# Performance work log

Measured on AMD Instinct MI355X. Metric: run time of the kernel, lower is better.

## Reference

```python
import jax, jax.numpy as jnp
import numpy as np

B, C, D, H, W = 8, 256, 128, 64, 64


def setup_inputs() -> dict:
    key = jax.random.key(0)
    ks = jax.random.split(key, 7)
    s = 1.0 / np.sqrt(C)
    return {
        "q": jax.random.normal(ks[0], (B, C, H, W), dtype=jnp.float32),
        "k": jax.random.normal(ks[1], (B, C, H, W), dtype=jnp.float32),
        "v": jax.random.normal(ks[2], (B, C, H, W), dtype=jnp.float32),
        "W_theta": jax.random.normal(ks[3], (D, C), dtype=jnp.float32) * s,
        "W_phi": jax.random.normal(ks[4], (D, C), dtype=jnp.float32) * s,
        "W_g": jax.random.normal(ks[5], (D, C), dtype=jnp.float32) * s,
        "W_out": jax.random.normal(ks[6], (C, D), dtype=jnp.float32) * (1.0 / np.sqrt(D)),
    }


def reference(q, k, v, W_theta, W_phi, W_g, W_out):
    # 1x1 conv projections (no bias) == channel matmuls
    b, c, h, w = q.shape
    d = W_theta.shape[0]
    n = h * w
    qp = jnp.einsum('bchw,dc->bhwd', q, W_theta).reshape(b, n, d)   # [B,N,d]
    kp = jnp.einsum('bchw,dc->bhwd', k, W_phi).reshape(b, n, d)     # [B,N,d]
    vp = jnp.einsum('bchw,dc->bhwd', v, W_g).reshape(b, n, d)       # [B,N,d]
    # embedded_gaussian: scores / sqrt(d), softmax over dim=1 (query axis!)
    scores = jnp.einsum('bnd,bmd->bnm', qp, kp) / jnp.sqrt(jnp.asarray(d, qp.dtype))
    attn = jax.nn.softmax(scores, axis=1)                           # NOTE: axis=1, matches torch dim=1
    out = jnp.einsum('bnm,bmd->bnd', attn, vp).reshape(b, h, w, d)  # [B,H,W,d]
    out = jnp.einsum('bhwd,cd->bchw', out, W_out)                   # conv_out 1x1
    return v + out
```

## Files before the change

kernel.cpp:

```cpp
#include <hip/hip_runtime.h>
#include <stdint.h>

#define B_ 8
#define C_ 256
#define D_ 128
#define N_ 4096

typedef __bf16 bf16x8 __attribute__((ext_vector_type(8)));
typedef uint16_t u16x8 __attribute__((ext_vector_type(8)));
typedef uint16_t u16x4 __attribute__((ext_vector_type(4)));
typedef float f32x4 __attribute__((ext_vector_type(4)));
typedef uint32_t u32x2 __attribute__((ext_vector_type(2)));

__device__ inline uint16_t f2bf(float x) {
    union { float f; uint32_t u; } v; v.f = x;
    uint32_t u = v.u;
    return (uint16_t)((u + 0x7FFFu + ((u >> 16) & 1u)) >> 16);
}

__device__ inline float bf2f(uint16_t v) {
    union { uint32_t u; float f; } x; x.u = (uint32_t)v << 16; return x.f;
}

__device__ inline uint32_t pkbf(float lo, float hi) {
    __bf16 l = (__bf16)lo, h = (__bf16)hi;
    uint16_t lu = __builtin_bit_cast(uint16_t, l);
    uint16_t hu = __builtin_bit_cast(uint16_t, h);
    return ((uint32_t)hu << 16) | (uint32_t)lu;
}

__device__ inline float dexp2(float x) { return __builtin_amdgcn_exp2f(x); }

__global__ __launch_bounds__(256) void prep_weights(
    const float* __restrict__ wt, const float* __restrict__ wp,
    const float* __restrict__ wg, const float* __restrict__ wo,
    uint16_t* __restrict__ bwt, uint16_t* __restrict__ bwp,
    uint16_t* __restrict__ bwg, uint16_t* __restrict__ bwo)
{
    int i = blockIdx.x * 256 + threadIdx.x;
    const float scale = 0.127517431f;
    bwt[i] = f2bf(wt[i] * scale);
    bwp[i] = f2bf(wp[i]);
    bwg[i] = f2bf(wg[i]);
    bwo[i] = f2bf(wo[i]);
}

__global__ __launch_bounds__(256) void proj_kernel(
    const float* __restrict__ q, const float* __restrict__ k, const float* __restrict__ v,
    const uint16_t* __restrict__ bwt, const uint16_t* __restrict__ bwp, const uint16_t* __restrict__ bwg,
    uint16_t* __restrict__ qp, uint16_t* __restrict__ kp, uint16_t* __restrict__ vpT)
{
    const int which = blockIdx.z;
    const float* src = (which == 0) ? q : ((which == 1) ? k : v);
    const uint16_t* w = (which == 0) ? bwt : ((which == 1) ? bwp : bwg);
    const int b   = blockIdx.y;
    const int n0  = blockIdx.x * 64;
    const int wav = threadIdx.x >> 6;
    const int lane = threadIdx.x & 63;
    const int col = lane & 15;
    const int quad = lane >> 4;
    const int n = n0 + wav * 16 + col;

    const float* srcb = src + (size_t)b * C_ * N_;

    f32x4 acc[8];
#pragma unroll
    for (int mf = 0; mf < 8; ++mf) acc[mf] = (f32x4){0.f, 0.f, 0.f, 0.f};

    for (int kc = 0; kc < 8; ++kc) {
        const int cbase = kc * 32 + quad * 8;
        u16x8 bb;
#pragma unroll
        for (int j = 0; j < 8; ++j)
            bb[j] = f2bf(srcb[(size_t)(cbase + j) * N_ + n]);
        bf16x8 bfrag = __builtin_bit_cast(bf16x8, bb);
#pragma unroll
        for (int mf = 0; mf < 8; ++mf) {
            bf16x8 afrag = *(const bf16x8*)(w + (size_t)(mf * 16 + col) * C_ + cbase);
            acc[mf] = __builtin_amdgcn_mfma_f32_16x16x32_bf16(afrag, bfrag, acc[mf], 0, 0, 0);
        }
    }

    if (which < 2) {
        uint16_t* dst = (which == 0) ? qp : kp;
        uint16_t* base = dst + ((size_t)b * N_ + n) * D_;
#pragma unroll
        for (int mf = 0; mf < 8; ++mf) {
            u16x4 pk;
#pragma unroll
            for (int r = 0; r < 4; ++r) pk[r] = f2bf(acc[mf][r]);
            *(u16x4*)(base + mf * 16 + quad * 4) = pk;
        }
    } else {
        uint16_t* base = vpT + (size_t)b * D_ * N_;
#pragma unroll
        for (int mf = 0; mf < 8; ++mf)
#pragma unroll
            for (int r = 0; r < 4; ++r) {
                int d = mf * 16 + quad * 4 + r;
                base[(size_t)d * N_ + n] = f2bf(acc[mf][r]);
            }
    }
}

__global__ __launch_bounds__(256) void pass1_denom(
    const uint16_t* __restrict__ qp, const uint16_t* __restrict__ kp,
    float* __restrict__ part)
{
    const int b  = blockIdx.x & 7;
    const int mt = (blockIdx.x >> 3) & 31;
    const int ns = blockIdx.x >> 8;
    const int m0 = mt * 128;
    const int wav = threadIdx.x >> 6;
    const int lane = threadIdx.x & 63;
    const int c = lane & 15;
    const int q = lane >> 4;

    const uint16_t* qpb = qp + (size_t)b * N_ * D_;
    const uint16_t* kpb = kp + (size_t)b * N_ * D_;

    bf16x8 bfr[8][4];
#pragma unroll
    for (int mf = 0; mf < 8; ++mf)
#pragma unroll
        for (int kc = 0; kc < 4; ++kc)
            bfr[mf][kc] = *(const bf16x8*)(kpb + (size_t)(m0 + mf * 16 + c) * D_ + kc * 32 + q * 8);

    float colsum[8];
#pragma unroll
    for (int mf = 0; mf < 8; ++mf) colsum[mf] = 0.f;

    for (int it = 0; it < 32; ++it) {
        const int nbase = ns * 2048 + it * 64 + wav * 16;
        bf16x8 afr[4];
#pragma unroll
        for (int kc = 0; kc < 4; ++kc)
            afr[kc] = *(const bf16x8*)(qpb + (size_t)(nbase + c) * D_ + kc * 32 + q * 8);
#pragma unroll
        for (int mf = 0; mf < 8; ++mf) {
            f32x4 acc = (f32x4){0.f, 0.f, 0.f, 0.f};
#pragma unroll
            for (int kc = 0; kc < 4; ++kc)
                acc = __builtin_amdgcn_mfma_f32_16x16x32_bf16(afr[kc], bfr[mf][kc], acc, 0, 0, 0);
#pragma unroll
            for (int r = 0; r < 4; ++r)
                colsum[mf] += dexp2(acc[r]);
        }
    }

    __shared__ float cs[4][128];
#pragma unroll
    for (int mf = 0; mf < 8; ++mf) {
        float s = colsum[mf];
        s += __shfl_down(s, 16, 64);
        s += __shfl_down(s, 32, 64);
        if (q == 0) cs[wav][mf * 16 + c] = s;
    }
    __syncthreads();
    if (threadIdx.x < 128) {
        float s = cs[0][threadIdx.x] + cs[1][threadIdx.x] + cs[2][threadIdx.x] + cs[3][threadIdx.x];
        part[((size_t)ns * 8 + b) * N_ + m0 + threadIdx.x] = s;
    }
}

__global__ __launch_bounds__(256) void scale_vpt(
    const float* __restrict__ part, uint16_t* __restrict__ vpT)
{
    const size_t base = ((size_t)blockIdx.x * 256 + threadIdx.x) * 8;
    const int b = (int)(base >> 19);
    const int m = (int)(base & (N_ - 1));
    const float* p0 = part + (size_t)b * N_ + m;
    const float* p1 = part + (size_t)(8 + b) * N_ + m;
    u16x8 v = *(const u16x8*)(vpT + base);
    u16x8 r;
#pragma unroll
    for (int j = 0; j < 8; ++j) {
        float inv = __builtin_amdgcn_rcpf(p0[j] + p1[j]);
        r[j] = f2bf(bf2f(v[j]) * inv);
    }
    *(u16x8*)(vpT + base) = r;
}

__global__ __launch_bounds__(256, 2) void pass2_attn(
    const uint16_t* __restrict__ qp, const uint16_t* __restrict__ kp,
    const uint16_t* __restrict__ vpT,
    uint16_t* __restrict__ ob0, uint16_t* __restrict__ ob1,
    uint16_t* __restrict__ ob2, uint16_t* __restrict__ ob3)
{
    const int b   = blockIdx.x & 7;
    const int qtr = (blockIdx.x >> 3) & 3;
    const int nsb = blockIdx.x >> 5;
    const int wav = threadIdx.x >> 6;
    const int lane = threadIdx.x & 63;
    const int c = lane & 15;
    const int q = lane >> 4;
    const int ntile = nsb * 256 + wav * 64;

    const uint16_t* qpb = qp + (size_t)b * N_ * D_;
    const uint16_t* kpb = kp + (size_t)b * N_ * D_;
    const uint16_t* vtb = vpT + (size_t)b * D_ * N_;

    __shared__ __align__(16) uint16_t stage[2][8192];
    __shared__ __align__(16) uint16_t plds[4][4][16][72];

#define STAGE(bufidx, m0_)                                                          \
    {                                                                               \
        uint16_t* lb = &stage[bufidx][0];                                           \
        _Pragma("unroll")                                                           \
        for (int j = 0; j < 4; ++j) {                                               \
            const int fid = wav * 4 + j;                                            \
            const uint16_t* g;                                                      \
            uint16_t* ld;                                                           \
            if (fid < 8) {                                                          \
                const int P = fid * 64 + lane;                                      \
                const int mm = P >> 4, js = P & 15;                                 \
                const int jj = js ^ (mm & 7);                                       \
                g = kpb + (size_t)((m0_) + mm) * D_ + jj * 8;                       \
                ld = lb + fid * 512;                                                \
            } else {                                                                \
                const int P = (fid - 8) * 64 + lane;                                \
                const int dd = P >> 2, js = P & 3;                                  \
                const int jj = js ^ ((dd >> 1) & 3);                                \
                g = vtb + (size_t)dd * N_ + (m0_) + jj * 8;                         \
                ld = lb + 4096 + (fid - 8) * 512;                                   \
            }                                                                       \
            __builtin_amdgcn_global_load_lds(                                       \
                (const __attribute__((address_space(1))) unsigned int*)g,           \
                (__attribute__((address_space(3))) unsigned int*)ld,                \
                16, 0, 0);                                                          \
        }                                                                           \
    }

    bf16x8 qfr[4][4];
#pragma unroll
    for (int nf = 0; nf < 4; ++nf)
#pragma unroll
        for (int kc = 0; kc < 4; ++kc)
            qfr[nf][kc] = *(const bf16x8*)(qpb + (size_t)(ntile + nf * 16 + c) * D_ + kc * 32 + q * 8);

    f32x4 oacc[4][8];
#pragma unroll
    for (int nf = 0; nf < 4; ++nf)
#pragma unroll
        for (int df = 0; df < 8; ++df) oacc[nf][df] = (f32x4){0.f, 0.f, 0.f, 0.f};

    const int mstart = qtr * (N_ / 4);
    STAGE(0, mstart);
    __syncthreads();

    for (int ch = 0; ch < 32; ++ch) {
        const int m0 = mstart + ch * 32;
        const int cur = ch & 1;
        STAGE(cur ^ 1, mstart + ((ch + 1) & 31) * 32);

        const uint16_t* sb = &stage[cur][0];

        bf16x8 kf[2][4];
#pragma unroll
        for (int mf = 0; mf < 2; ++mf)
#pragma unroll
            for (int kc = 0; kc < 4; ++kc) {
                const int js = (kc * 4 + q) ^ (c & 7);
                kf[mf][kc] = *(const bf16x8*)(sb + (mf * 16 + c) * 128 + js * 8);
            }

        __builtin_amdgcn_s_setprio(1);
#pragma unroll
        for (int nf = 0; nf < 4; ++nf) {
            f32x4 s0 = (f32x4){0.f, 0.f, 0.f, 0.f};
            f32x4 s1 = (f32x4){0.f, 0.f, 0.f, 0.f};
#pragma unroll
            for (int kc = 0; kc < 4; ++kc)
                s0 = __builtin_amdgcn_mfma_f32_16x16x32_bf16(kf[0][kc], qfr[nf][kc], s0, 0, 0, 0);
#pragma unroll
            for (int kc = 0; kc < 4; ++kc)
                s1 = __builtin_amdgcn_mfma_f32_16x16x32_bf16(kf[1][kc], qfr[nf][kc], s1, 0, 0, 0);
            uint32_t p00 = pkbf(dexp2(s0[0]), dexp2(s0[1]));
            uint32_t p01 = pkbf(dexp2(s0[2]), dexp2(s0[3]));
            uint32_t p10 = pkbf(dexp2(s1[0]), dexp2(s1[1]));
            uint32_t p11 = pkbf(dexp2(s1[2]), dexp2(s1[3]));
            uint16_t* row = &plds[wav][nf][c][0];
            *(u32x2*)(row + 4 * q)      = (u32x2){p00, p01};
            *(u32x2*)(row + 16 + 4 * q) = (u32x2){p10, p11};
        }
        __builtin_amdgcn_s_setprio(0);

        const int vjs = q ^ ((c >> 1) & 3);
        bf16x8 vf[8];
#pragma unroll
        for (int df = 0; df < 8; ++df)
            vf[df] = *(const bf16x8*)(sb + 4096 + (df * 16 + c) * 32 + vjs * 8);

        bf16x8 pf[4];
#pragma unroll
        for (int nf = 0; nf < 4; ++nf)
            pf[nf] = *(const bf16x8*)(&plds[wav][nf][c][8 * q]);

        __builtin_amdgcn_s_setprio(1);
#pragma unroll
        for (int nf = 0; nf < 4; ++nf)
#pragma unroll
            for (int df = 0; df < 8; ++df)
                oacc[nf][df] = __builtin_amdgcn_mfma_f32_16x16x32_bf16(pf[nf], vf[df], oacc[nf][df], 0, 0, 0);
        __builtin_amdgcn_s_setprio(0);

        __syncthreads();
    }
#undef STAGE

    uint16_t* obq = (qtr == 0) ? ob0 : (qtr == 1) ? ob1 : (qtr == 2) ? ob2 : ob3;
#pragma unroll
    for (int nf = 0; nf < 4; ++nf) {
        uint16_t* ob = obq + ((size_t)b * N_ + ntile + nf * 16) * D_;
#pragma unroll
        for (int df = 0; df < 8; ++df)
#pragma unroll
            for (int r = 0; r < 4; ++r)
                ob[(size_t)(q * 4 + r) * D_ + df * 16 + c] = f2bf(oacc[nf][df][r]);
    }
}

__global__ __launch_bounds__(256) void pass3_out(
    const uint16_t* __restrict__ ob0, const uint16_t* __restrict__ ob1,
    const uint16_t* __restrict__ ob2, const uint16_t* __restrict__ ob3,
    const uint16_t* __restrict__ bwo,
    const float* __restrict__ v, float* __restrict__ out)
{
    const int b  = blockIdx.y;
    const int n0 = blockIdx.x * 64;
    const int wav = threadIdx.x >> 6;
    const int lane = threadIdx.x & 63;
    const int col = lane & 15;
    const int quad = lane >> 4;
    const int n = n0 + wav * 16 + col;

    const float* vb = v + (size_t)b * C_ * N_;
    float* outb = out + (size_t)b * C_ * N_;
    const size_t off = ((size_t)b * N_ + n) * D_;

    bf16x8 f0[4], f1[4], f2[4], f3[4];
#pragma unroll
    for (int kc = 0; kc < 4; ++kc) {
        f0[kc] = *(const bf16x8*)(ob0 + off + kc * 32 + quad * 8);
        f1[kc] = *(const bf16x8*)(ob1 + off + kc * 32 + quad * 8);
        f2[kc] = *(const bf16x8*)(ob2 + off + kc * 32 + quad * 8);
        f3[kc] = *(const bf16x8*)(ob3 + off + kc * 32 + quad * 8);
    }

#pragma unroll
    for (int cf = 0; cf < 16; ++cf) {
        f32x4 acc = (f32x4){0.f, 0.f, 0.f, 0.f};
#pragma unroll
        for (int kc = 0; kc < 4; ++kc) {
            bf16x8 afr = *(const bf16x8*)(bwo + (size_t)(cf * 16 + col) * D_ + kc * 32 + quad * 8);
            acc = __builtin_amdgcn_mfma_f32_16x16x32_bf16(afr, f0[kc], acc, 0, 0, 0);
            acc = __builtin_amdgcn_mfma_f32_16x16x32_bf16(afr, f1[kc], acc, 0, 0, 0);
            acc = __builtin_amdgcn_mfma_f32_16x16x32_bf16(afr, f2[kc], acc, 0, 0, 0);
            acc = __builtin_amdgcn_mfma_f32_16x16x32_bf16(afr, f3[kc], acc, 0, 0, 0);
        }
#pragma unroll
        for (int r = 0; r < 4; ++r) {
            const int cc = cf * 16 + quad * 4 + r;
            const size_t idx = (size_t)cc * N_ + n;
            outb[idx] = vb[idx] + acc[r];
        }
    }
}

extern "C" void kernel_launch(void* const* d_in, const int* in_sizes, int n_in,
                              void* d_out, int out_size, void* d_ws, size_t ws_size,
                              hipStream_t stream) {
    const float* q  = (const float*)d_in[0];
    const float* k  = (const float*)d_in[1];
    const float* v  = (const float*)d_in[2];
    const float* wt = (const float*)d_in[3];
    const float* wp = (const float*)d_in[4];
    const float* wg = (const float*)d_in[5];
    const float* wo = (const float*)d_in[6];
    float* out = (float*)d_out;

    const size_t PROJ = (size_t)B_ * N_ * D_;
    uint16_t* qp  = (uint16_t*)d_ws;
    uint16_t* kp  = qp + PROJ;
    uint16_t* vpT = kp + PROJ;
    uint16_t* ob0 = vpT + PROJ;
    uint16_t* ob1 = ob0 + PROJ;
    uint16_t* ob2 = ob1 + PROJ;
    uint16_t* ob3 = ob2 + PROJ;
    uint16_t* bwt = ob3 + PROJ;
    uint16_t* bwp = bwt + (size_t)D_ * C_;
    uint16_t* bwg = bwp + (size_t)D_ * C_;
    uint16_t* bwo = bwg + (size_t)D_ * C_;
    float* part = (float*)ob0;

    prep_weights<<<dim3(128), 256, 0, stream>>>(wt, wp, wg, wo, bwt, bwp, bwg, bwo);
    proj_kernel<<<dim3(N_ / 64, B_, 3), 256, 0, stream>>>(q, k, v, bwt, bwp, bwg, qp, kp, vpT);
    pass1_denom<<<dim3(512), 256, 0, stream>>>(qp, kp, part);
    scale_vpt<<<dim3(2048), 256, 0, stream>>>(part, vpT);
    pass2_attn<<<dim3(512), 256, 0, stream>>>(qp, kp, vpT, ob0, ob1, ob2, ob3);
    pass3_out<<<dim3(N_ / 64, B_), 256, 0, stream>>>(ob0, ob1, ob2, ob3, bwo, v, out);
}
```

Baseline: 364.6 us.

## Switch attention pass to 32x32 MFMA with register-resident P and log-bias normalization

Rewrites the attention pass to use 32x32x16 bf16 MFMA tiles instead of 16x16x32, using permlane32_swap to turn the score accumulator layout into the P operand layout in registers. This removes the per-wave LDS round trip for P. The per-key softmax denominator is now folded in as a -log2 bias added to the score accumulators before exp2, replacing the separate pass that rescaled V. The V-scaling kernel is replaced by a tiny log kernel, and partial sums move to their own workspace region. The cost is larger accumulator fragments, which raise register pressure at 2 blocks per CU, plus a per-chunk bias load.

```diff
diff --git a/kernel.cpp b/kernel.cpp
--- a/kernel.cpp
+++ b/kernel.cpp
@@ -10,16 +10,14 @@
 typedef uint16_t u16x8 __attribute__((ext_vector_type(8)));
 typedef uint16_t u16x4 __attribute__((ext_vector_type(4)));
 typedef float f32x4 __attribute__((ext_vector_type(4)));
-typedef uint32_t u32x2 __attribute__((ext_vector_type(2)));
+typedef float f32x16 __attribute__((ext_vector_type(16)));
+typedef uint32_t u32x4 __attribute__((ext_vector_type(4)));
+typedef unsigned int uiv2 __attribute__((ext_vector_type(2)));
 
 __device__ inline uint16_t f2bf(float x) {
     union { float f; uint32_t u; } v; v.f = x;
     uint32_t u = v.u;
     return (uint16_t)((u + 0x7FFFu + ((u >> 16) & 1u)) >> 16);
-}
-
-__device__ inline float bf2f(uint16_t v) {
-    union { uint32_t u; float f; } x; x.u = (uint32_t)v << 16; return x.f;
 }
 
 __device__ inline uint32_t pkbf(float lo, float hi) {
@@ -163,27 +161,16 @@
     }
 }
 
-__global__ __launch_bounds__(256) void scale_vpt(
-    const float* __restrict__ part, uint16_t* __restrict__ vpT)
-{
-    const size_t base = ((size_t)blockIdx.x * 256 + threadIdx.x) * 8;
-    const int b = (int)(base >> 19);
-    const int m = (int)(base & (N_ - 1));
-    const float* p0 = part + (size_t)b * N_ + m;
-    const float* p1 = part + (size_t)(8 + b) * N_ + m;
-    u16x8 v = *(const u16x8*)(vpT + base);
-    u16x8 r;
-#pragma unroll
-    for (int j = 0; j < 8; ++j) {
-        float inv = __builtin_amdgcn_rcpf(p0[j] + p1[j]);
-        r[j] = f2bf(bf2f(v[j]) * inv);
-    }
-    *(u16x8*)(vpT + base) = r;
+__global__ __launch_bounds__(256) void neglog2_kernel(
+    const float* __restrict__ part, float* __restrict__ l2i)
+{
+    int i = blockIdx.x * 256 + threadIdx.x;
+    l2i[i] = -__builtin_amdgcn_logf(part[i] + part[32768 + i]);
 }
 
 __global__ __launch_bounds__(256, 2) void pass2_attn(
     const uint16_t* __restrict__ qp, const uint16_t* __restrict__ kp,
-    const uint16_t* __restrict__ vpT,
+    const uint16_t* __restrict__ vpT, const float* __restrict__ l2i,
     uint16_t* __restrict__ ob0, uint16_t* __restrict__ ob1,
     uint16_t* __restrict__ ob2, uint16_t* __restrict__ ob3)
 {
@@ -192,16 +179,16 @@
     const int nsb = blockIdx.x >> 5;
     const int wav = threadIdx.x >> 6;
     const int lane = threadIdx.x & 63;
-    const int c = lane & 15;
-    const int q = lane >> 4;
+    const int l31 = lane & 31;
+    const int hl  = lane >> 5;
     const int ntile = nsb * 256 + wav * 64;
 
     const uint16_t* qpb = qp + (size_t)b * N_ * D_;
     const uint16_t* kpb = kp + (size_t)b * N_ * D_;
     const uint16_t* vtb = vpT + (size_t)b * D_ * N_;
+    const float* l2b = l2i + (size_t)b * N_;
 
     __shared__ __align__(16) uint16_t stage[2][8192];
-    __shared__ __align__(16) uint16_t plds[4][4][16][72];
 
 #define STAGE(bufidx, m0_)                                                          \
     {                                                                               \
@@ -231,18 +218,20 @@
         }                                                                           \
     }
 
-    bf16x8 qfr[4][4];
-#pragma unroll
-    for (int nf = 0; nf < 4; ++nf)
-#pragma unroll
-        for (int kc = 0; kc < 4; ++kc)
-            qfr[nf][kc] = *(const bf16x8*)(qpb + (size_t)(ntile + nf * 16 + c) * D_ + kc * 32 + q * 8);
-
-    f32x4 oacc[4][8];
-#pragma unroll
-    for (int nf = 0; nf < 4; ++nf)
-#pragma unroll
-        for (int df = 0; df < 8; ++df) oacc[nf][df] = (f32x4){0.f, 0.f, 0.f, 0.f};
+    bf16x8 qfr[2][8];
+#pragma unroll
+    for (int nt = 0; nt < 2; ++nt)
+#pragma unroll
+        for (int ks = 0; ks < 8; ++ks)
+            qfr[nt][ks] = *(const bf16x8*)(qpb + (size_t)(ntile + nt * 32 + l31) * D_ + ks * 16 + hl * 8);
+
+    f32x16 oacc[2][4];
+#pragma unroll
+    for (int nt = 0; nt < 2; ++nt)
+#pragma unroll
+        for (int dt = 0; dt < 4; ++dt)
+#pragma unroll
+            for (int r = 0; r < 16; ++r) oacc[nt][dt][r] = 0.f;
 
     const int mstart = qtr * (N_ / 4);
     STAGE(0, mstart);
@@ -255,53 +244,53 @@
 
         const uint16_t* sb = &stage[cur][0];
 
-        bf16x8 kf[2][4];
-#pragma unroll
-        for (int mf = 0; mf < 2; ++mf)
-#pragma unroll
-            for (int kc = 0; kc < 4; ++kc) {
-                const int js = (kc * 4 + q) ^ (c & 7);
-                kf[mf][kc] = *(const bf16x8*)(sb + (mf * 16 + c) * 128 + js * 8);
-            }
-
+        f32x4 bias[4];
+#pragma unroll
+        for (int g = 0; g < 4; ++g)
+            bias[g] = *(const f32x4*)(l2b + m0 + 8 * g + 4 * hl);
+
+        uint32_t pf[2][2][4];
         __builtin_amdgcn_s_setprio(1);
 #pragma unroll
-        for (int nf = 0; nf < 4; ++nf) {
-            f32x4 s0 = (f32x4){0.f, 0.f, 0.f, 0.f};
-            f32x4 s1 = (f32x4){0.f, 0.f, 0.f, 0.f};
-#pragma unroll
-            for (int kc = 0; kc < 4; ++kc)
-                s0 = __builtin_amdgcn_mfma_f32_16x16x32_bf16(kf[0][kc], qfr[nf][kc], s0, 0, 0, 0);
-#pragma unroll
-            for (int kc = 0; kc < 4; ++kc)
-                s1 = __builtin_amdgcn_mfma_f32_16x16x32_bf16(kf[1][kc], qfr[nf][kc], s1, 0, 0, 0);
-            uint32_t p00 = pkbf(dexp2(s0[0]), dexp2(s0[1]));
-            uint32_t p01 = pkbf(dexp2(s0[2]), dexp2(s0[3]));
-            uint32_t p10 = pkbf(dexp2(s1[0]), dexp2(s1[1]));
-            uint32_t p11 = pkbf(dexp2(s1[2]), dexp2(s1[3]));
-            uint16_t* row = &plds[wav][nf][c][0];
-            *(u32x2*)(row + 4 * q)      = (u32x2){p00, p01};
-            *(u32x2*)(row + 16 + 4 * q) = (u32x2){p10, p11};
+        for (int nt = 0; nt < 2; ++nt) {
+            f32x16 sa;
+#pragma unroll
+            for (int r = 0; r < 16; ++r) sa[r] = bias[r >> 2][r & 3];
+#pragma unroll
+            for (int ks = 0; ks < 8; ++ks) {
+                bf16x8 kf = *(const bf16x8*)(sb + l31 * 128 + ((2 * ks + hl) ^ (l31 & 7)) * 8);
+                sa = __builtin_amdgcn_mfma_f32_32x32x16_bf16(kf, qfr[nt][ks], sa, 0, 0, 0);
+            }
+#pragma unroll
+            for (int k2 = 0; k2 < 2; ++k2) {
+                const int rb = k2 * 8;
+                uint32_t X = pkbf(dexp2(sa[rb + 0]), dexp2(sa[rb + 1]));
+                uint32_t Y = pkbf(dexp2(sa[rb + 2]), dexp2(sa[rb + 3]));
+                uint32_t Z = pkbf(dexp2(sa[rb + 4]), dexp2(sa[rb + 5]));
+                uint32_t W = pkbf(dexp2(sa[rb + 6]), dexp2(sa[rb + 7]));
+                uiv2 xz = __builtin_amdgcn_permlane32_swap(X, Z, false, false);
+                uiv2 yw = __builtin_amdgcn_permlane32_swap(Y, W, false, false);
+                pf[nt][k2][0] = xz[0];
+                pf[nt][k2][1] = yw[0];
+                pf[nt][k2][2] = xz[1];
+                pf[nt][k2][3] = yw[1];
+            }
         }
         __builtin_amdgcn_s_setprio(0);
 
-        const int vjs = q ^ ((c >> 1) & 3);
-        bf16x8 vf[8];
-#pragma unroll
-        for (int df = 0; df < 8; ++df)
-            vf[df] = *(const bf16x8*)(sb + 4096 + (df * 16 + c) * 32 + vjs * 8);
-
-        bf16x8 pf[4];
-#pragma unroll
-        for (int nf = 0; nf < 4; ++nf)
-            pf[nf] = *(const bf16x8*)(&plds[wav][nf][c][8 * q]);
-
+        const int vsw = (l31 >> 1) & 3;
         __builtin_amdgcn_s_setprio(1);
 #pragma unroll
-        for (int nf = 0; nf < 4; ++nf)
-#pragma unroll
-            for (int df = 0; df < 8; ++df)
-                oacc[nf][df] = __builtin_amdgcn_mfma_f32_16x16x32_bf16(pf[nf], vf[df], oacc[nf][df], 0, 0, 0);
+        for (int k2 = 0; k2 < 2; ++k2) {
+#pragma unroll
+            for (int dt = 0; dt < 4; ++dt) {
+                bf16x8 vf = *(const bf16x8*)(sb + 4096 + (dt * 32 + l31) * 32 + ((2 * k2 + hl) ^ vsw) * 8);
+                bf16x8 pa0 = __builtin_bit_cast(bf16x8, *(u32x4*)&pf[0][k2][0]);
+                bf16x8 pa1 = __builtin_bit_cast(bf16x8, *(u32x4*)&pf[1][k2][0]);
+                oacc[0][dt] = __builtin_amdgcn_mfma_f32_32x32x16_bf16(pa0, vf, oacc[0][dt], 0, 0, 0);
+                oacc[1][dt] = __builtin_amdgcn_mfma_f32_32x32x16_bf16(pa1, vf, oacc[1][dt], 0, 0, 0);
+            }
+        }
         __builtin_amdgcn_s_setprio(0);
 
         __syncthreads();
@@ -310,14 +299,14 @@
 
     uint16_t* obq = (qtr == 0) ? ob0 : (qtr == 1) ? ob1 : (qtr == 2) ? ob2 : ob3;
 #pragma unroll
-    for (int nf = 0; nf < 4; ++nf) {
-        uint16_t* ob = obq + ((size_t)b * N_ + ntile + nf * 16) * D_;
-#pragma unroll
-        for (int df = 0; df < 8; ++df)
-#pragma unroll
-            for (int r = 0; r < 4; ++r)
-                ob[(size_t)(q * 4 + r) * D_ + df * 16 + c] = f2bf(oacc[nf][df][r]);
-    }
+    for (int nt = 0; nt < 2; ++nt)
+#pragma unroll
+        for (int dt = 0; dt < 4; ++dt)
+#pragma unroll
+            for (int r = 0; r < 16; ++r) {
+                const int n = ntile + nt * 32 + (r & 3) + 8 * (r >> 2) + 4 * hl;
+                obq[((size_t)b * N_ + n) * D_ + dt * 32 + l31] = f2bf(oacc[nt][dt][r]);
+            }
 }
 
 __global__ __launch_bounds__(256) void pass3_out(
@@ -391,12 +380,13 @@
     uint16_t* bwp = bwt + (size_t)D_ * C_;
     uint16_t* bwg = bwp + (size_t)D_ * C_;
     uint16_t* bwo = bwg + (size_t)D_ * C_;
-    float* part = (float*)ob0;
+    float* part   = (float*)(bwo + (size_t)D_ * C_);
+    float* l2i    = part + (size_t)2 * 8 * N_;
 
     prep_weights<<<dim3(128), 256, 0, stream>>>(wt, wp, wg, wo, bwt, bwp, bwg, bwo);
     proj_kernel<<<dim3(N_ / 64, B_, 3), 256, 0, stream>>>(q, k, v, bwt, bwp, bwg, qp, kp, vpT);
     pass1_denom<<<dim3(512), 256, 0, stream>>>(qp, kp, part);
-    scale_vpt<<<dim3(2048), 256, 0, stream>>>(part, vpT);
-    pass2_attn<<<dim3(512), 256, 0, stream>>>(qp, kp, vpT, ob0, ob1, ob2, ob3);
+    neglog2_kernel<<<dim3(128), 256, 0, stream>>>(part, l2i);
+    pass2_attn<<<dim3(512), 256, 0, stream>>>(qp, kp, vpT, l2i, ob0, ob1, ob2, ob3);
     pass3_out<<<dim3(N_ / 64, B_), 256, 0, stream>>>(ob0, ob1, ob2, ob3, bwo, v, out);
 }
```

Result: slower. 422.0 us (+15.8%).

## Fold softmax denominator into score bias via log, drop V rescale kernel

Applied to the files above, without the earlier changes.

The full-tensor scale_vpt pass, which read and rewrote vpT divided by the column sums, is removed. A tiny kernel instead computes -log2 of each column's denominator, and pass2 uses it as the initial MFMA accumulator, so exp2 directly yields normalized probabilities. The projection kernel also unrolls its channel loop, preloads weight fragments, and packs bf16 conversions in pairs. This adds a small bias load per chunk in pass2 and moves the partial-sum buffer to its own workspace region.

```diff
diff --git a/kernel.cpp b/kernel.cpp
--- a/kernel.cpp
+++ b/kernel.cpp
@@ -67,18 +67,24 @@
 #pragma unroll
     for (int mf = 0; mf < 8; ++mf) acc[mf] = (f32x4){0.f, 0.f, 0.f, 0.f};
 
+#pragma unroll
     for (int kc = 0; kc < 8; ++kc) {
         const int cbase = kc * 32 + quad * 8;
-        u16x8 bb;
+        bf16x8 afr[8];
+#pragma unroll
+        for (int mf = 0; mf < 8; ++mf)
+            afr[mf] = *(const bf16x8*)(w + (size_t)(mf * 16 + col) * C_ + cbase);
+        float x[8];
 #pragma unroll
         for (int j = 0; j < 8; ++j)
-            bb[j] = f2bf(srcb[(size_t)(cbase + j) * N_ + n]);
-        bf16x8 bfrag = __builtin_bit_cast(bf16x8, bb);
-#pragma unroll
-        for (int mf = 0; mf < 8; ++mf) {
-            bf16x8 afrag = *(const bf16x8*)(w + (size_t)(mf * 16 + col) * C_ + cbase);
-            acc[mf] = __builtin_amdgcn_mfma_f32_16x16x32_bf16(afrag, bfrag, acc[mf], 0, 0, 0);
-        }
+            x[j] = srcb[(size_t)(cbase + j) * N_ + n];
+        u32x2 blo = (u32x2){pkbf(x[0], x[1]), pkbf(x[2], x[3])};
+        u32x2 bhi = (u32x2){pkbf(x[4], x[5]), pkbf(x[6], x[7])};
+        uint32_t bw[4] = {blo[0], blo[1], bhi[0], bhi[1]};
+        bf16x8 bfrag = __builtin_bit_cast(bf16x8, bw);
+#pragma unroll
+        for (int mf = 0; mf < 8; ++mf)
+            acc[mf] = __builtin_amdgcn_mfma_f32_16x16x32_bf16(afr[mf], bfrag, acc[mf], 0, 0, 0);
     }
 
     if (which < 2) {
@@ -86,10 +92,8 @@
         uint16_t* base = dst + ((size_t)b * N_ + n) * D_;
 #pragma unroll
         for (int mf = 0; mf < 8; ++mf) {
-            u16x4 pk;
-#pragma unroll
-            for (int r = 0; r < 4; ++r) pk[r] = f2bf(acc[mf][r]);
-            *(u16x4*)(base + mf * 16 + quad * 4) = pk;
+            u32x2 pk = (u32x2){pkbf(acc[mf][0], acc[mf][1]), pkbf(acc[mf][2], acc[mf][3])};
+            *(u32x2*)(base + mf * 16 + quad * 4) = pk;
         }
     } else {
         uint16_t* base = vpT + (size_t)b * D_ * N_;
@@ -163,27 +167,16 @@
     }
 }
 
-__global__ __launch_bounds__(256) void scale_vpt(
-    const float* __restrict__ part, uint16_t* __restrict__ vpT)
-{
-    const size_t base = ((size_t)blockIdx.x * 256 + threadIdx.x) * 8;
-    const int b = (int)(base >> 19);
-    const int m = (int)(base & (N_ - 1));
-    const float* p0 = part + (size_t)b * N_ + m;
-    const float* p1 = part + (size_t)(8 + b) * N_ + m;
-    u16x8 v = *(const u16x8*)(vpT + base);
-    u16x8 r;
-#pragma unroll
-    for (int j = 0; j < 8; ++j) {
-        float inv = __builtin_amdgcn_rcpf(p0[j] + p1[j]);
-        r[j] = f2bf(bf2f(v[j]) * inv);
-    }
-    *(u16x8*)(vpT + base) = r;
+__global__ __launch_bounds__(256) void neglog2_kernel(
+    const float* __restrict__ part, float* __restrict__ l2i)
+{
+    int i = blockIdx.x * 256 + threadIdx.x;
+    l2i[i] = -__builtin_amdgcn_logf(part[i] + part[32768 + i]);
 }
 
 __global__ __launch_bounds__(256, 2) void pass2_attn(
     const uint16_t* __restrict__ qp, const uint16_t* __restrict__ kp,
-    const uint16_t* __restrict__ vpT,
+    const uint16_t* __restrict__ vpT, const float* __restrict__ l2i,
     uint16_t* __restrict__ ob0, uint16_t* __restrict__ ob1,
     uint16_t* __restrict__ ob2, uint16_t* __restrict__ ob3)
 {
@@ -199,6 +192,7 @@
     const uint16_t* qpb = qp + (size_t)b * N_ * D_;
     const uint16_t* kpb = kp + (size_t)b * N_ * D_;
     const uint16_t* vtb = vpT + (size_t)b * D_ * N_;
+    const float* l2b = l2i + (size_t)b * N_;
 
     __shared__ __align__(16) uint16_t stage[2][8192];
     __shared__ __align__(16) uint16_t plds[4][4][16][72];
@@ -255,6 +249,9 @@
 
         const uint16_t* sb = &stage[cur][0];
 
+        const f32x4 bias0 = *(const f32x4*)(l2b + m0 + 4 * q);
+        const f32x4 bias1 = *(const f32x4*)(l2b + m0 + 16 + 4 * q);
+
         bf16x8 kf[2][4];
 #pragma unroll
         for (int mf = 0; mf < 2; ++mf)
@@ -267,8 +264,8 @@
         __builtin_amdgcn_s_setprio(1);
 #pragma unroll
         for (int nf = 0; nf < 4; ++nf) {
-            f32x4 s0 = (f32x4){0.f, 0.f, 0.f, 0.f};
-            f32x4 s1 = (f32x4){0.f, 0.f, 0.f, 0.f};
+            f32x4 s0 = bias0;
+            f32x4 s1 = bias1;
 #pragma unroll
             for (int kc = 0; kc < 4; ++kc)
                 s0 = __builtin_amdgcn_mfma_f32_16x16x32_bf16(kf[0][kc], qfr[nf][kc], s0, 0, 0, 0);
@@ -391,12 +388,13 @@
     uint16_t* bwp = bwt + (size_t)D_ * C_;
     uint16_t* bwg = bwp + (size_t)D_ * C_;
     uint16_t* bwo = bwg + (size_t)D_ * C_;
-    float* part = (float*)ob0;
+    float* part   = (float*)(bwo + (size_t)D_ * C_);
+    float* l2i    = part + (size_t)2 * 8 * N_;
 
     prep_weights<<<dim3(128), 256, 0, stream>>>(wt, wp, wg, wo, bwt, bwp, bwg, bwo);
     proj_kernel<<<dim3(N_ / 64, B_, 3), 256, 0, stream>>>(q, k, v, bwt, bwp, bwg, qp, kp, vpT);
     pass1_denom<<<dim3(512), 256, 0, stream>>>(qp, kp, part);
-    scale_vpt<<<dim3(2048), 256, 0, stream>>>(part, vpT);
-    pass2_attn<<<dim3(512), 256, 0, stream>>>(qp, kp, vpT, ob0, ob1, ob2, ob3);
+    neglog2_kernel<<<dim3(128), 256, 0, stream>>>(part, l2i);
+    pass2_attn<<<dim3(512), 256, 0, stream>>>(qp, kp, vpT, l2i, ob0, ob1, ob2, ob3);
     pass3_out<<<dim3(N_ / 64, B_), 256, 0, stream>>>(ob0, ob1, ob2, ob3, bwo, v, out);
 }
```

Result: no change. 365.2 us (+0.2%).
